# Optimization experiments

Measured on AMD Instinct MI355X. Metric: run time of the kernel, lower is better.

The kernel has to match this reference:

```python
import jax, jax.numpy as jnp
import numpy as np

LEAK = 0.1

def _l2n(x):
    return x / (jnp.linalg.norm(x) + 1e-12)

def _sn_weight(W, u):
    # torch spectral_norm: one power iteration from buffer u, u/v detached,
    # grad flows through W via sigma = u' W v.
    v = jax.lax.stop_gradient(_l2n(W.T @ u))
    u2 = jax.lax.stop_gradient(_l2n(W @ v))
    sigma = u2 @ (W @ v)
    return W / sigma

def _conv1x1(x, W, b):
    # x: (B,C,H,W), W: (O,C) -> (B,O,H,W)
    return jnp.einsum('oc,bchw->bohw', W, x) + b[None, :, None, None]

def _sn_layer(x, W, b, u):
    return jax.nn.leaky_relu(_conv1x1(x, _sn_weight(W, u), b), LEAK)

def _attention(x, qW, qb, kW, kb, vW, vb, gamma):
    B, C, H, Wd = x.shape
    N = H * Wd
    q = _conv1x1(x, qW, qb).reshape(B, -1, N)   # (B, C//8, N)
    k = _conv1x1(x, kW, kb).reshape(B, -1, N)   # (B, C//8, N)
    v = _conv1x1(x, vW, vb).reshape(B, C, N)    # (B, C, N)
    # energy[b,n,m] = sum_c q[b,c,n] * k[b,c,m]  (query^T key)
    energy = jnp.einsum('bcn,bcm->bnm', q, k)
    amap = jax.nn.softmax(energy, axis=-1)
    # aw[b,c,m] = sum_n v[b,c,n] * amap[b,m,n]   (bmm(v, amap^T))
    aw = jnp.einsum('bcn,bmn->bcm', v, amap).reshape(B, C, H, Wd)
    return gamma * aw + x


def setup_inputs() -> dict:
    key = jax.random.key(0)
    ks = iter(jax.random.split(key, 64))
    def nrm(shape, s=0.05):
        return jax.random.normal(next(ks), shape, jnp.float32) * s
    d = {'input': jax.random.normal(next(ks), (4, 6, 64, 64), jnp.float32)}
    dims = [(6, 64), (64, 128), (128, 256), (256, 512), (512, 1)]
    for i, (cin, cout) in enumerate(dims, 1):
        d[f'W{i}'] = nrm((cout, cin))
        d[f'b{i}'] = nrm((cout,))
        d[f'u{i}'] = _l2n(jax.random.normal(next(ks), (cout,), jnp.float32))
    for tag, C in (('a1', 256), ('a2', 512)):
        d[f'{tag}_qW'] = nrm((C // 8, C)); d[f'{tag}_qb'] = nrm((C // 8,))
        d[f'{tag}_kW'] = nrm((C // 8, C)); d[f'{tag}_kb'] = nrm((C // 8,))
        d[f'{tag}_vW'] = nrm((C, C));      d[f'{tag}_vb'] = nrm((C,))
        d[f'{tag}_gamma'] = jnp.full((1,), 0.1, jnp.float32)
    return d


def reference(input, W1, b1, u1, W2, b2, u2, W3, b3, u3, W4, b4, u4, W5, b5, u5,
              a1_qW, a1_qb, a1_kW, a1_kb, a1_vW, a1_vb, a1_gamma,
              a2_qW, a2_qb, a2_kW, a2_kb, a2_vW, a2_vb, a2_gamma):
    out = _sn_layer(input, W1, b1, u1)
    out = _sn_layer(out, W2, b2, u2)
    out = _sn_layer(out, W3, b3, u3)
    out = _attention(out, a1_qW, a1_qb, a1_kW, a1_kb, a1_vW, a1_vb, a1_gamma)
    out = _sn_layer(out, W4, b4, u4)
    out = _attention(out, a2_qW, a2_qb, a2_kW, a2_kb, a2_vW, a2_vb, a2_gamma)
    out = _sn_layer(out, W5, b5, u5)
    return out.squeeze()  # (B, H, W)
```

## Files before the change

### kernel.cpp

```cpp
#include <hip/hip_runtime.h>
#include <math.h>

#define N_PIX 4096
#define BATCH 4
#define LOG2E 1.4426950408889634f

typedef __bf16 bf16x8 __attribute__((ext_vector_type(8)));
typedef __bf16 bf16x4v __attribute__((ext_vector_type(4)));
typedef float f32x4 __attribute__((ext_vector_type(4)));

__device__ __forceinline__ unsigned pack4_fp8(float a, float b, float c, float d) {
    unsigned p = __builtin_amdgcn_cvt_pk_fp8_f32(a, b, 0, false);
    p = __builtin_amdgcn_cvt_pk_fp8_f32(c, d, p, true);
    return p;
}
__device__ __forceinline__ uint8_t to_fp8(float v) {
    return (uint8_t)(__builtin_amdgcn_cvt_pk_fp8_f32(v, v, 0, false) & 0xff);
}

struct SigP {
    const float* W[5];
    const float* u[5];
    int O[5];
    int C[5];
};

__device__ __forceinline__ void sig_map(int bid, int& L, int& ch) {
    if (bid == 0)      { L = 0; ch = 0; }
    else if (bid < 3)  { L = 1; ch = bid - 1; }
    else if (bid < 7)  { L = 2; ch = bid - 3; }
    else if (bid < 15) { L = 3; ch = bid - 7; }
    else               { L = 4; ch = 0; }
}

__global__ __launch_bounds__(256)
void sigma_p1(SigP p, float* __restrict__ ybuf) {
    __shared__ float ush[64];
    int L, ch;
    sig_map(blockIdx.x, L, ch);
    const float* W = p.W[L];
    const float* u = p.u[L];
    int O = p.O[L], C = p.C[L];
    int o0 = ch * 64;
    int no = O - o0; if (no > 64) no = 64;
    int t = threadIdx.x;
    if (t < 64) ush[t] = (t < no) ? u[o0 + t] : 0.f;
    __syncthreads();
    for (int c = t; c < C; c += 256) {
        float a = 0.f;
        for (int o = 0; o < no; ++o) a += W[(size_t)(o0 + o) * C + c] * ush[o];
        atomicAdd(&ybuf[L * 512 + c], a);
    }
}

__global__ __launch_bounds__(256)
void sigma_p2(SigP p, const float* __restrict__ ybuf,
              float* __restrict__ S1, float* __restrict__ S2) {
    __shared__ float ysh[512];
    int L, ch;
    sig_map(blockIdx.x, L, ch);
    const float* W = p.W[L];
    int O = p.O[L], C = p.C[L];
    int o0 = ch * 64;
    int o_hi = o0 + 64; if (o_hi > O) o_hi = O;
    int t = threadIdx.x;
    int lane = t & 63, w = t >> 6;
    for (int c = t; c < C; c += 256) ysh[c] = ybuf[L * 512 + c];
    __syncthreads();

    if (ch == 0) {
        float s = 0.f;
        for (int c = t; c < C; c += 256) s += ysh[c] * ysh[c];
        #pragma unroll
        for (int off = 1; off < 64; off <<= 1) s += __shfl_xor(s, off);
        if (lane == 0) atomicAdd(&S1[L], s);
    }

    float sq = 0.f;
    for (int i = 0; i < 16; ++i) {
        int o = o0 + w * 16 + i;
        if (o >= o_hi) break;
        float a = 0.f;
        for (int c = lane; c < C; c += 64) a += W[(size_t)o * C + c] * ysh[c];
        #pragma unroll
        for (int off = 1; off < 64; off <<= 1) a += __shfl_xor(a, off);
        if (lane == 0) sq += a * a;
    }
    if (lane == 0) atomicAdd(&S2[L], sq);
}

__global__ __launch_bounds__(256)
void wsplit_kernel(const float* __restrict__ W, const float* __restrict__ iv,
                   float scale, int C, __bf16* __restrict__ out) {
    int o = blockIdx.x;
    float s = (iv ? iv[0] : 1.f) * scale;
    for (int c = threadIdx.x; c < C; c += 256) {
        float wv = W[(size_t)o * C + c] * s;
        __bf16 hi = (__bf16)wv;
        float lo = wv - (float)hi;
        out[(size_t)o * 2 * C + c] = hi;
        out[(size_t)o * 2 * C + C + c] = (__bf16)lo;
    }
}

__global__ __launch_bounds__(256)
void concat_bias(const float* __restrict__ qb1, const float* __restrict__ kb1,
                 const float* __restrict__ qb2, const float* __restrict__ kb2,
                 float* __restrict__ bb,
                 const float* __restrict__ S1, const float* __restrict__ S2,
                 float* __restrict__ sig) {
    int t = threadIdx.x;
    if (t < 32) bb[t] = qb1[t] * LOG2E;
    else if (t < 64) bb[t] = kb1[t - 32];
    else if (t < 128) bb[t] = qb2[t - 64] * LOG2E;
    else if (t < 192) bb[t] = kb2[t - 128];
    else if (t >= 224 && t < 229) {
        int L = t - 224;
        float rinv = 1.f / (sqrtf(S1[L]) + 1e-12f);
        float ns2 = rinv * rinv * S2[L];
        float sg = ns2 / (sqrtf(ns2) + 1e-12f);
        sig[L] = 1.f / sg;
    }
}

__global__ __launch_bounds__(256)
void conv_f32_kernel(const float* __restrict__ x, const float* __restrict__ W,
                     const float* __restrict__ bias, const float* __restrict__ sig,
                     float* __restrict__ out, int C, int O, int lrelu) {
    __shared__ float Ws[16][68];
    __shared__ float Xs[16][68];
    int t = threadIdx.x;
    int tx = t & 15, ty = t >> 4;
    int b = blockIdx.z;
    int n0 = blockIdx.x * 64, o0 = blockIdx.y * 64;
    float acc[4][4] = {};
    const float* xb = x + (size_t)b * C * N_PIX;
    for (int c0 = 0; c0 < C; c0 += 16) {
        #pragma unroll
        for (int i = 0; i < 4; ++i) {
            int e = t + i * 256;
            int o = e >> 4, c = e & 15;
            float wv = 0.f;
            if (o0 + o < O && c0 + c < C) wv = W[(size_t)(o0 + o) * C + c0 + c];
            Ws[c][o] = wv;
        }
        #pragma unroll
        for (int i = 0; i < 4; ++i) {
            int e = t + i * 256;
            int c = e >> 6, n = e & 63;
            float xv = 0.f;
            if (c0 + c < C) xv = xb[(size_t)(c0 + c) * N_PIX + n0 + n];
            Xs[c][n] = xv;
        }
        __syncthreads();
        #pragma unroll
        for (int cc = 0; cc < 16; ++cc) {
            float4 wv = *(const float4*)&Ws[cc][ty * 4];
            float4 xv = *(const float4*)&Xs[cc][tx * 4];
            float wa[4] = {wv.x, wv.y, wv.z, wv.w};
            float xa[4] = {xv.x, xv.y, xv.z, xv.w};
            #pragma unroll
            for (int i = 0; i < 4; ++i)
                #pragma unroll
                for (int j = 0; j < 4; ++j)
                    acc[i][j] += wa[i] * xa[j];
        }
        __syncthreads();
    }
    float ivv = sig ? sig[0] : 1.f;
    for (int i = 0; i < 4; ++i) {
        int o = o0 + ty * 4 + i;
        if (o >= O) break;
        float bv = bias[o];
        float vres[4];
        #pragma unroll
        for (int j = 0; j < 4; ++j) {
            float v = acc[i][j] * ivv + bv;
            if (lrelu) v = (v > 0.f) ? v : 0.1f * v;
            vres[j] = v;
        }
        *(float4*)&out[((size_t)b * O + o) * N_PIX + n0 + tx * 4] =
            make_float4(vres[0], vres[1], vres[2], vres[3]);
    }
}

__global__ __launch_bounds__(256)
void tsplit64_kernel(const float* __restrict__ in, __bf16* __restrict__ out) {
    __shared__ float tile[64 * 65];
    int t = threadIdx.x;
    int n0 = blockIdx.x * 64, b = blockIdx.y;
    for (int e = t; e < 64 * 64; e += 256) {
        int c = e >> 6, n = e & 63;
        tile[n * 65 + c] = in[((size_t)b * 64 + c) * N_PIX + n0 + n];
    }
    __syncthreads();
    for (int e = t; e < 64 * 64; e += 256) {
        int n = e >> 6, c = e & 63;
        float v = tile[n * 65 + c];
        __bf16 hi = (__bf16)v;
        size_t base = ((size_t)b * N_PIX + n0 + n) * 128;
        out[base + c] = hi;
        out[base + 64 + c] = (__bf16)(v - (float)hi);
    }
}

template <int WO, int WN, int MF, int MODE, int IN_F32, int LRELU>
__global__ __launch_bounds__(256)
void mfma_conv(const void* __restrict__ xt, const __bf16* __restrict__ wsp,
               const float* __restrict__ bias, float bscale,
               void* __restrict__ outp, int C, int O) {
    constexpr int NT_BLK = WN * 128;
    constexpr int OT_BLK = WO * 16 * MF;
    __shared__ __bf16 Ws[OT_BLK * 72];
    __shared__ __bf16 Xs[NT_BLK * 72];
    int t = threadIdx.x;
    int lane = t & 63, w = t >> 6;
    int l15 = lane & 15, quad = lane >> 4;
    int wo = w / WN, wn = w % WN;
    int b = blockIdx.z;
    int n0b = blockIdx.x * NT_BLK, o0b = blockIdx.y * OT_BLK;

    f32x4 acc[MF][8] = {};

    for (int c0 = 0; c0 < C; c0 += 32) {
        __syncthreads();
        for (int e = t; e < OT_BLK * 8; e += 256) {
            int row = e >> 3, part = e & 7;
            size_t src = (size_t)(o0b + row) * 2 * C +
                         (part < 4 ? c0 + part * 8 : C + c0 + (part - 4) * 8);
            int dst = row * 72 + (part < 4 ? part * 8 : 32 + (part - 4) * 8);
            *(uint4*)&Ws[dst] = *(const uint4*)&wsp[src];
        }
        if (IN_F32) {
            const float* xf = (const float*)xt;
            for (int e = t; e < NT_BLK * 8; e += 256) {
                int row = e >> 3, part = e & 7;
                float4 v = *(const float4*)&xf[((size_t)b * N_PIX + n0b + row) * C + c0 + part * 4];
                bf16x4v hi, lo;
                float va[4] = {v.x, v.y, v.z, v.w};
                #pragma unroll
                for (int j = 0; j < 4; ++j) {
                    hi[j] = (__bf16)va[j];
                    lo[j] = (__bf16)(va[j] - (float)hi[j]);
                }
                *(bf16x4v*)&Xs[row * 72 + part * 4] = hi;
                *(bf16x4v*)&Xs[row * 72 + 32 + part * 4] = lo;
            }
        } else {
            const __bf16* xb = (const __bf16*)xt;
            for (int e = t; e < NT_BLK * 8; e += 256) {
                int row = e >> 3, part = e & 7;
                size_t src = ((size_t)b * N_PIX + n0b + row) * 2 * C +
                             (part < 4 ? c0 + part * 8 : C + c0 + (part - 4) * 8);
                int dst = row * 72 + (part < 4 ? part * 8 : 32 + (part - 4) * 8);
                *(uint4*)&Xs[dst] = *(const uint4*)&xb[src];
            }
        }
        __syncthreads();

        bf16x8 ah[MF], al[MF];
        #pragma unroll
        for (int mf = 0; mf < MF; ++mf) {
            int base = (wo * 16 * MF + mf * 16 + l15) * 72 + quad * 8;
            ah[mf] = *(const bf16x8*)&Ws[base];
            al[mf] = *(const bf16x8*)&Ws[base + 32];
        }
        #pragma unroll
        for (int nt = 0; nt < 8; ++nt) {
            int bbase = (wn * 128 + nt * 16 + l15) * 72 + quad * 8;
            bf16x8 bh = *(const bf16x8*)&Xs[bbase];
            bf16x8 bl = *(const bf16x8*)&Xs[bbase + 32];
            #pragma unroll
            for (int mf = 0; mf < MF; ++mf) {
                acc[mf][nt] = __builtin_amdgcn_mfma_f32_16x16x32_bf16(ah[mf], bh, acc[mf][nt], 0, 0, 0);
                acc[mf][nt] = __builtin_amdgcn_mfma_f32_16x16x32_bf16(ah[mf], bl, acc[mf][nt], 0, 0, 0);
                acc[mf][nt] = __builtin_amdgcn_mfma_f32_16x16x32_bf16(al[mf], bh, acc[mf][nt], 0, 0, 0);
            }
        }
    }

    float bv[MF][4];
    #pragma unroll
    for (int mf = 0; mf < MF; ++mf)
        #pragma unroll
        for (int r = 0; r < 4; ++r)
            bv[mf][r] = bias[o0b + wo * 16 * MF + mf * 16 + quad * 4 + r] * bscale;

    #pragma unroll
    for (int mf = 0; mf < MF; ++mf)
        #pragma unroll
        for (int nt = 0; nt < 8; ++nt) {
            int n = n0b + wn * 128 + nt * 16 + l15;
            float val[4];
            #pragma unroll
            for (int r = 0; r < 4; ++r) {
                float v = acc[mf][nt][r] + bv[mf][r];
                if (LRELU) v = (v > 0.f) ? v : 0.1f * v;
                val[r] = v;
            }
            int obase = o0b + wo * 16 * MF + mf * 16 + quad * 4;
            if (MODE == 1) {
                uint8_t* ob = (uint8_t*)outp;
                #pragma unroll
                for (int r = 0; r < 4; ++r)
                    ob[((size_t)b * O + obase + r) * N_PIX + n] = to_fp8(val[r]);
            } else if (MODE == 2) {
                __bf16* ob = (__bf16*)outp;
                bf16x4v hv, lv;
                #pragma unroll
                for (int r = 0; r < 4; ++r) {
                    hv[r] = (__bf16)val[r];
                    lv[r] = (__bf16)(val[r] - (float)hv[r]);
                }
                size_t rb = ((size_t)b * N_PIX + n) * 2 * O + obase;
                *(bf16x4v*)&ob[rb] = hv;
                *(bf16x4v*)&ob[rb + O] = lv;
            } else {
                __bf16* ob = (__bf16*)outp;
                bf16x4v hv;
                #pragma unroll
                for (int r = 0; r < 4; ++r) hv[r] = (__bf16)val[r];
                *(bf16x4v*)&ob[((size_t)b * N_PIX + n) * O + obase] = hv;
            }
        }
}

template <int CQ, int KITER>
__global__ __launch_bounds__(256)
void s_gemm3(const __bf16* __restrict__ qt, const __bf16* __restrict__ kt,
             uint8_t* __restrict__ S, int QSTR) {
    constexpr int NKK = CQ / 32;
    __shared__ uint8_t Ss[2][128 * 144];
    int t = threadIdx.x;
    int lane = t & 63, w = t >> 6;
    int l15 = lane & 15, quad = lane >> 4;
    int kbase = blockIdx.x * KITER * 128, q0 = blockIdx.y * 128, b = blockIdx.z;

    bf16x8 qf[8][NKK];
    #pragma unroll
    for (int nt = 0; nt < 8; ++nt)
        #pragma unroll
        for (int kk = 0; kk < NKK; ++kk)
            qf[nt][kk] = *(const bf16x8*)&qt[((size_t)b * N_PIX + q0 + nt * 16 + l15) * QSTR + kk * 32 + quad * 8];

    for (int ki = 0; ki < KITER; ++ki) {
        int k0 = kbase + ki * 128;
        int cur = ki & 1;
        bf16x8 kf[2][NKK];
        #pragma unroll
        for (int mf = 0; mf < 2; ++mf)
            #pragma unroll
            for (int kk = 0; kk < NKK; ++kk)
                kf[mf][kk] = *(const bf16x8*)&kt[((size_t)b * N_PIX + k0 + w * 32 + mf * 16 + l15) * QSTR + kk * 32 + quad * 8];

        #pragma unroll
        for (int nt = 0; nt < 8; ++nt) {
            f32x4 a[2] = {};
            #pragma unroll
            for (int kk = 0; kk < NKK; ++kk)
                #pragma unroll
                for (int mf = 0; mf < 2; ++mf)
                    a[mf] = __builtin_amdgcn_mfma_f32_16x16x32_bf16(kf[mf][kk], qf[nt][kk], a[mf], 0, 0, 0);
            #pragma unroll
            for (int mf = 0; mf < 2; ++mf) {
                unsigned p = pack4_fp8(exp2f(a[mf][0]), exp2f(a[mf][1]),
                                       exp2f(a[mf][2]), exp2f(a[mf][3]));
                *(unsigned*)&Ss[cur][(nt * 16 + l15) * 144 + w * 32 + mf * 16 + quad * 4] = p;
            }
        }
        __syncthreads();
        int ql = t >> 1, kh = (t & 1) * 64;
        size_t row = ((size_t)b * N_PIX + q0 + ql) * (size_t)N_PIX + k0 + kh;
        #pragma unroll
        for (int j = 0; j < 4; ++j)
            *(uint4*)&S[row + j * 16] = *(const uint4*)&Ss[cur][ql * 144 + kh + j * 16];
    }
}

typedef __attribute__((address_space(1))) const void* gas1_t;
typedef __attribute__((address_space(3))) void* las3_t;

template <int NT, int QROWS>
__global__ __launch_bounds__(1024)
void pv_gemm13(const uint8_t* __restrict__ E, const uint8_t* __restrict__ vg,
               const __bf16* __restrict__ xin2,
               const float* __restrict__ gamma, float* __restrict__ out, int C) {
    constexpr int NQS = QROWS / 32;
    constexpr int NCS = 16 / NQS;
    constexpr int CCH = NT * 16 * NCS;
    constexpr int NPAIR = (N_PIX / QROWS) * BATCH;
    __shared__ uint8_t PshA[QROWS * 128];
    __shared__ uint8_t PshB[QROWS * 128];
    __shared__ uint8_t VshA[CCH * 128];
    __shared__ uint8_t VshB[CCH * 128];
    int t = threadIdx.x;
    int lane = t & 63, w = t >> 6;
    int l15 = lane & 15, quad = lane >> 4;
    int qs = w % NQS, cs = w / NQS;
    int bid = blockIdx.x;
    int pair = bid % NPAIR, cblk = bid / NPAIR;
    int qi = pair >> 2, b = pair & 3;
    int q0 = qi * QROWS, c0 = cblk * CCH;
    const uint8_t* Pb = E + ((size_t)b * N_PIX + q0) * (size_t)N_PIX;
    const uint8_t* Vb = vg + ((size_t)b * C + c0) * (size_t)N_PIX;

    int r8 = lane >> 3;
    int cgl = (lane & 7) ^ r8;

    const long ONES = 0x3838383838383838L;

    f32x4 acc[2][NT] = {};
    f32x4 acc_s[2] = {};

    auto stage = [&](uint8_t* Ps, uint8_t* Vs, int k0) {
        #pragma unroll
        for (int ch = 0; ch < QROWS / 128; ++ch) {
            int row0 = w * (QROWS / 16) + ch * 8;
            const uint8_t* g = Pb + (size_t)(row0 + r8) * N_PIX + k0 + cgl * 16;
            __builtin_amdgcn_global_load_lds((gas1_t)g, (las3_t)&Ps[row0 * 128], 16, 0, 0);
        }
        static_assert(CCH / 8 == 16, "V staging assumes 16 chunks");
        {
            int row0 = w * 8;
            const uint8_t* g = Vb + (size_t)(row0 + r8) * N_PIX + k0 + cgl * 16;
            __builtin_amdgcn_global_load_lds((gas1_t)g, (las3_t)&Vs[row0 * 128], 16, 0, 0);
        }
    };

    auto compute = [&](const uint8_t* Ps, const uint8_t* Vs) {
        #pragma unroll
        for (int kk = 0; kk < 4; ++kk) {
            long pa[2];
            #pragma unroll
            for (int mf = 0; mf < 2; ++mf) {
                int row = qs * 32 + mf * 16 + l15;
                int cg = (2 * kk + (quad >> 1)) ^ (row & 7);
                pa[mf] = *(const long*)&Ps[row * 128 + cg * 16 + (quad & 1) * 8];
            }
            #pragma unroll
            for (int mf = 0; mf < 2; ++mf)
                acc_s[mf] = __builtin_amdgcn_mfma_f32_16x16x32_fp8_fp8(pa[mf], ONES, acc_s[mf], 0, 0, 0);
            #pragma unroll
            for (int nt = 0; nt < NT; ++nt) {
                int row = cs * (NT * 16) + nt * 16 + l15;
                int cg = (2 * kk + (quad >> 1)) ^ (row & 7);
                long vf = *(const long*)&Vs[row * 128 + cg * 16 + (quad & 1) * 8];
                #pragma unroll
                for (int mf = 0; mf < 2; ++mf)
                    acc[mf][nt] = __builtin_amdgcn_mfma_f32_16x16x32_fp8_fp8(pa[mf], vf, acc[mf][nt], 0, 0, 0);
            }
        }
    };

    stage(PshA, VshA, 0);
    __syncthreads();

    for (int k0 = 0; k0 < N_PIX; k0 += 256) {
        stage(PshB, VshB, k0 + 128);
        compute(PshA, VshA);
        __syncthreads();
        if (k0 + 256 < N_PIX) stage(PshA, VshA, k0 + 256);
        compute(PshB, VshB);
        __syncthreads();
    }

    float g = gamma[0];
    #pragma unroll
    for (int mf = 0; mf < 2; ++mf)
        #pragma unroll
        for (int r = 0; r < 4; ++r) {
            int ql = qs * 32 + mf * 16 + quad * 4 + r;
            int q = q0 + ql;
            float gil = g / acc_s[mf][r];
            size_t xrb = ((size_t)b * N_PIX + q) * 2 * C;
            size_t orb = ((size_t)b * N_PIX + q) * C;
            #pragma unroll
            for (int nt = 0; nt < NT; ++nt) {
                int c = c0 + cs * (NT * 16) + nt * 16 + l15;
                float xr = (float)xin2[xrb + c] + (float)xin2[xrb + C + c];
                out[orb + c] = gil * acc[mf][nt][r] + xr;
            }
        }
}

__global__ __launch_bounds__(256)
void l5_kernel(const float* __restrict__ h, const float* __restrict__ W5,
               const float* __restrict__ b5, const float* __restrict__ sig,
               float* __restrict__ out) {
    int t = threadIdx.x;
    int lane = t & 63, w = t >> 6;
    int p = blockIdx.x * 4 + w;
    const float* row = h + (size_t)p * 512;
    float4 a0 = *(const float4*)&row[lane * 8];
    float4 a1 = *(const float4*)&row[lane * 8 + 4];
    float4 w0 = *(const float4*)&W5[lane * 8];
    float4 w1 = *(const float4*)&W5[lane * 8 + 4];
    float s = a0.x * w0.x + a0.y * w0.y + a0.z * w0.z + a0.w * w0.w +
              a1.x * w1.x + a1.y * w1.y + a1.z * w1.z + a1.w * w1.w;
    #pragma unroll
    for (int off = 1; off < 64; off <<= 1) s += __shfl_xor(s, off);
    if (lane == 0) {
        float v = sig[0] * s + b5[0];
        out[p] = (v > 0.f) ? v : 0.1f * v;
    }
}

extern "C" void kernel_launch(void* const* d_in, const int* in_sizes, int n_in,
                              void* d_out, int out_size, void* d_ws, size_t ws_size,
                              hipStream_t stream) {
    const float* x   = (const float*)d_in[0];
    const float* W1  = (const float*)d_in[1];
    const float* b1  = (const float*)d_in[2];
    const float* u1  = (const float*)d_in[3];
    const float* W2  = (const float*)d_in[4];
    const float* b2  = (const float*)d_in[5];
    const float* u2  = (const float*)d_in[6];
    const float* W3  = (const float*)d_in[7];
    const float* b3  = (const float*)d_in[8];
    const float* u3  = (const float*)d_in[9];
    const float* W4  = (const float*)d_in[10];
    const float* b4  = (const float*)d_in[11];
    const float* u4  = (const float*)d_in[12];
    const float* W5  = (const float*)d_in[13];
    const float* b5  = (const float*)d_in[14];
    const float* u5  = (const float*)d_in[15];
    const float* a1_qW = (const float*)d_in[16];
    const float* a1_qb = (const float*)d_in[17];
    const float* a1_kW = (const float*)d_in[18];
    const float* a1_kb = (const float*)d_in[19];
    const float* a1_vW = (const float*)d_in[20];
    const float* a1_vb = (const float*)d_in[21];
    const float* a1_g  = (const float*)d_in[22];
    const float* a2_qW = (const float*)d_in[23];
    const float* a2_qb = (const float*)d_in[24];
    const float* a2_kW = (const float*)d_in[25];
    const float* a2_kb = (const float*)d_in[26];
    const float* a2_vW = (const float*)d_in[27];
    const float* a2_vb = (const float*)d_in[28];
    const float* a2_g  = (const float*)d_in[29];

    float* ws = (float*)d_ws;
    const size_t NF = (size_t)BATCH * N_PIX;
    float* sig    = ws;
    float* h1     = ws + 16;
    float* slabC  = h1 + NF * 64;
    float* slabS1 = slabC + NF * 512;
    float* slabS2 = slabS1 + NF * 256;
    float* qtf    = slabS2 + NF * 512;
    float* ktf    = qtf + NF * 32;
    float* wspf   = ktf + NF * 32;
    float* bbf    = wspf + 592000;
    float* ysig   = wspf + 592256;
    float* Sf     = wspf + 600000;

    __bf16* h1t = (__bf16*)slabS1;
    __bf16* h2t = (__bf16*)slabS2;
    __bf16* h3t = (__bf16*)slabS1;
    __bf16* h5t = (__bf16*)slabS2;
    float*  h4t = slabC;
    uint8_t* vb1 = (uint8_t*)(slabC + NF * 256);
    float*  h6t = slabC;
    uint8_t* vb2 = (uint8_t*)slabS1;
    __bf16* qkt = (__bf16*)qtf;
    __bf16* wsp = (__bf16*)wspf;
    uint8_t* Sbuf = (uint8_t*)Sf;

    float* ybuf = ysig;
    float* S1v  = ysig + 2560;
    float* S2v  = ysig + 2576;

    __bf16* wsL2  = wsp;
    __bf16* wsL3  = wsL2 + 16384;
    __bf16* wsL4  = wsL3 + 65536;
    __bf16* wsA1q = wsL4 + 262144;
    __bf16* wsA1k = wsA1q + 16384;
    __bf16* wsA1v = wsA1k + 16384;
    __bf16* wsA2q = wsA1v + 131072;
    __bf16* wsA2k = wsA2q + 65536;
    __bf16* wsA2v = wsA2k + 65536;

    dim3 blk(256);

    SigP sp;
    sp.W[0] = W1; sp.u[0] = u1; sp.O[0] = 64;  sp.C[0] = 6;
    sp.W[1] = W2; sp.u[1] = u2; sp.O[1] = 128; sp.C[1] = 64;
    sp.W[2] = W3; sp.u[2] = u3; sp.O[2] = 256; sp.C[2] = 128;
    sp.W[3] = W4; sp.u[3] = u4; sp.O[3] = 512; sp.C[3] = 256;
    sp.W[4] = W5; sp.u[4] = u5; sp.O[4] = 1;   sp.C[4] = 512;

    hipMemsetAsync(ysig, 0, 2592 * sizeof(float), stream);
    sigma_p1<<<dim3(16), blk, 0, stream>>>(sp, ybuf);
    sigma_p2<<<dim3(16), blk, 0, stream>>>(sp, ybuf, S1v, S2v);
    concat_bias<<<1, blk, 0, stream>>>(a1_qb, a1_kb, a2_qb, a2_kb, bbf, S1v, S2v, sig);

    wsplit_kernel<<<128, blk, 0, stream>>>(W2, sig + 1, 1.f, 64, wsL2);
    wsplit_kernel<<<256, blk, 0, stream>>>(W3, sig + 2, 1.f, 128, wsL3);
    wsplit_kernel<<<512, blk, 0, stream>>>(W4, sig + 3, 1.f, 256, wsL4);
    wsplit_kernel<<<32,  blk, 0, stream>>>(a1_qW, nullptr, LOG2E, 256, wsA1q);
    wsplit_kernel<<<32,  blk, 0, stream>>>(a1_kW, nullptr, 1.f, 256, wsA1k);
    wsplit_kernel<<<256, blk, 0, stream>>>(a1_vW, nullptr, 1.f, 256, wsA1v);
    wsplit_kernel<<<64,  blk, 0, stream>>>(a2_qW, nullptr, LOG2E, 512, wsA2q);
    wsplit_kernel<<<64,  blk, 0, stream>>>(a2_kW, nullptr, 1.f, 512, wsA2k);
    wsplit_kernel<<<512, blk, 0, stream>>>(a2_vW, nullptr, 1.f, 512, wsA2v);

    conv_f32_kernel<<<dim3(64, 1, 4), blk, 0, stream>>>(x, W1, b1, sig + 0, h1, 6, 64, 1);
    tsplit64_kernel<<<dim3(64, 4), blk, 0, stream>>>(h1, h1t);

    mfma_conv<4, 1, 1, 2, 0, 1><<<dim3(32, 2, 4), blk, 0, stream>>>(h1t, wsL2, b2, 1.f, h2t, 64, 128);
    mfma_conv<4, 1, 1, 2, 0, 1><<<dim3(32, 4, 4), blk, 0, stream>>>(h2t, wsL3, b3, 1.f, h3t, 128, 256);

    mfma_conv<2, 2, 1, 4, 0, 0><<<dim3(16, 2, 4), blk, 0, stream>>>(h3t, wsA1q, bbf, 1.f, qkt, 256, 64);
    mfma_conv<4, 1, 1, 1, 0, 0><<<dim3(32, 4, 4), blk, 0, stream>>>(h3t, wsA1v, a1_vb, 1.f, vb1, 256, 256);
    s_gemm3<32, 8><<<dim3(4, 32, 4), blk, 0, stream>>>(qkt, qkt + 32, Sbuf, 64);
    pv_gemm13<2, 128><<<dim3(256), dim3(1024), 0, stream>>>(Sbuf, vb1, h3t, a1_g, h4t, 256);

    mfma_conv<4, 1, 1, 2, 1, 1><<<dim3(32, 8, 4), blk, 0, stream>>>(h4t, wsL4, b4, 1.f, h5t, 256, 512);

    mfma_conv<2, 2, 1, 4, 0, 0><<<dim3(16, 4, 4), blk, 0, stream>>>(h5t, wsA2q, bbf + 64, 1.f, qkt, 512, 128);
    mfma_conv<4, 1, 1, 1, 0, 0><<<dim3(32, 8, 4), blk, 0, stream>>>(h5t, wsA2v, a2_vb, 1.f, vb2, 512, 512);
    s_gemm3<64, 8><<<dim3(4, 32, 4), blk, 0, stream>>>(qkt, qkt + 64, Sbuf, 128);
    pv_gemm13<4, 256><<<dim3(256), dim3(1024), 0, stream>>>(Sbuf, vb2, h5t, a2_g, h6t, 512);

    l5_kernel<<<4096, blk, 0, stream>>>(h6t, W5, b5, sig + 4, (float*)d_out);
}
```

Baseline: 526.4 us.

## Batch weight-split launches, fuse conv1 with transpose-split, drop memset and atomics

Measured after the change: 505.7 us, median of 2. -3.9%, faster.

```diff
diff --git a/kernel.cpp b/kernel.cpp
--- a/kernel.cpp
+++ b/kernel.cpp
@@ -49,23 +49,31 @@
     for (int c = t; c < C; c += 256) {
         float a = 0.f;
         for (int o = 0; o < no; ++o) a += W[(size_t)(o0 + o) * C + c] * ush[o];
-        atomicAdd(&ybuf[L * 512 + c], a);
+        ybuf[(size_t)blockIdx.x * 512 + c] = a;
     }
 }
 
 __global__ __launch_bounds__(256)
 void sigma_p2(SigP p, const float* __restrict__ ybuf,
-              float* __restrict__ S1, float* __restrict__ S2) {
+              float* __restrict__ S1, float* __restrict__ S2p) {
     __shared__ float ysh[512];
+    __shared__ float red[8];
     int L, ch;
     sig_map(blockIdx.x, L, ch);
+    const int baseT[5] = {0, 1, 3, 7, 15};
+    const int cntT[5]  = {1, 2, 4, 8, 1};
+    int base = baseT[L], cnt = cntT[L];
     const float* W = p.W[L];
     int O = p.O[L], C = p.C[L];
     int o0 = ch * 64;
     int o_hi = o0 + 64; if (o_hi > O) o_hi = O;
     int t = threadIdx.x;
     int lane = t & 63, w = t >> 6;
-    for (int c = t; c < C; c += 256) ysh[c] = ybuf[L * 512 + c];
+    for (int c = t; c < C; c += 256) {
+        float s = 0.f;
+        for (int i = 0; i < cnt; ++i) s += ybuf[(size_t)(base + i) * 512 + c];
+        ysh[c] = s;
+    }
     __syncthreads();
 
     if (ch == 0) {
@@ -73,7 +81,7 @@
         for (int c = t; c < C; c += 256) s += ysh[c] * ysh[c];
         #pragma unroll
         for (int off = 1; off < 64; off <<= 1) s += __shfl_xor(s, off);
-        if (lane == 0) atomicAdd(&S1[L], s);
+        if (lane == 0) red[w] = s;
     }
 
     float sq = 0.f;
@@ -86,20 +94,40 @@
         for (int off = 1; off < 64; off <<= 1) a += __shfl_xor(a, off);
         if (lane == 0) sq += a * a;
     }
-    if (lane == 0) atomicAdd(&S2[L], sq);
-}
-
-__global__ __launch_bounds__(256)
-void wsplit_kernel(const float* __restrict__ W, const float* __restrict__ iv,
-                   float scale, int C, __bf16* __restrict__ out) {
-    int o = blockIdx.x;
-    float s = (iv ? iv[0] : 1.f) * scale;
+    if (lane == 0) red[4 + w] = sq;
+    __syncthreads();
+    if (t == 0) {
+        if (ch == 0) S1[L] = red[0] + red[1] + red[2] + red[3];
+        S2p[blockIdx.x] = red[4] + red[5] + red[6] + red[7];
+    }
+}
+
+struct WsAll {
+    const float* W[9];
+    __bf16* out[9];
+    int C[9];
+    int sigidx[9];
+    float scale[9];
+    int end[9];
+};
+
+__global__ __launch_bounds__(256)
+void wsplit_all(WsAll p, const float* __restrict__ sig) {
+    int bid = blockIdx.x;
+    int s = 0;
+    #pragma unroll
+    for (int i = 0; i < 9; ++i)
+        if (bid >= p.end[i]) s = i + 1;
+    int o = bid - (s ? p.end[s - 1] : 0);
+    const float* W = p.W[s];
+    __bf16* out = p.out[s];
+    int C = p.C[s];
+    float sc = (p.sigidx[s] >= 0 ? sig[p.sigidx[s]] : 1.f) * p.scale[s];
     for (int c = threadIdx.x; c < C; c += 256) {
-        float wv = W[(size_t)o * C + c] * s;
+        float wv = W[(size_t)o * C + c] * sc;
         __bf16 hi = (__bf16)wv;
-        float lo = wv - (float)hi;
         out[(size_t)o * 2 * C + c] = hi;
-        out[(size_t)o * 2 * C + C + c] = (__bf16)lo;
+        out[(size_t)o * 2 * C + C + c] = (__bf16)(wv - (float)hi);
     }
 }
 
@@ -107,7 +135,7 @@
 void concat_bias(const float* __restrict__ qb1, const float* __restrict__ kb1,
                  const float* __restrict__ qb2, const float* __restrict__ kb2,
                  float* __restrict__ bb,
-                 const float* __restrict__ S1, const float* __restrict__ S2,
+                 const float* __restrict__ S1, const float* __restrict__ S2p,
                  float* __restrict__ sig) {
     int t = threadIdx.x;
     if (t < 32) bb[t] = qb1[t] * LOG2E;
@@ -116,82 +144,69 @@
     else if (t < 192) bb[t] = kb2[t - 128];
     else if (t >= 224 && t < 229) {
         int L = t - 224;
+        const int baseT[5] = {0, 1, 3, 7, 15};
+        const int cntT[5]  = {1, 2, 4, 8, 1};
+        float s2 = 0.f;
+        for (int i = 0; i < cntT[L]; ++i) s2 += S2p[baseT[L] + i];
         float rinv = 1.f / (sqrtf(S1[L]) + 1e-12f);
-        float ns2 = rinv * rinv * S2[L];
+        float ns2 = rinv * rinv * s2;
         float sg = ns2 / (sqrtf(ns2) + 1e-12f);
         sig[L] = 1.f / sg;
     }
 }
 
 __global__ __launch_bounds__(256)
-void conv_f32_kernel(const float* __restrict__ x, const float* __restrict__ W,
-                     const float* __restrict__ bias, const float* __restrict__ sig,
-                     float* __restrict__ out, int C, int O, int lrelu) {
+void conv1_kernel(const float* __restrict__ x, const float* __restrict__ W,
+                  const float* __restrict__ bias, const float* __restrict__ sig,
+                  __bf16* __restrict__ out) {
+    constexpr int C = 6;
     __shared__ float Ws[16][68];
     __shared__ float Xs[16][68];
+    __shared__ float tile[64 * 65];
     int t = threadIdx.x;
     int tx = t & 15, ty = t >> 4;
     int b = blockIdx.z;
-    int n0 = blockIdx.x * 64, o0 = blockIdx.y * 64;
+    int n0 = blockIdx.x * 64;
     float acc[4][4] = {};
     const float* xb = x + (size_t)b * C * N_PIX;
-    for (int c0 = 0; c0 < C; c0 += 16) {
-        #pragma unroll
-        for (int i = 0; i < 4; ++i) {
-            int e = t + i * 256;
-            int o = e >> 4, c = e & 15;
-            float wv = 0.f;
-            if (o0 + o < O && c0 + c < C) wv = W[(size_t)(o0 + o) * C + c0 + c];
-            Ws[c][o] = wv;
-        }
-        #pragma unroll
-        for (int i = 0; i < 4; ++i) {
-            int e = t + i * 256;
-            int c = e >> 6, n = e & 63;
-            float xv = 0.f;
-            if (c0 + c < C) xv = xb[(size_t)(c0 + c) * N_PIX + n0 + n];
-            Xs[c][n] = xv;
-        }
-        __syncthreads();
-        #pragma unroll
-        for (int cc = 0; cc < 16; ++cc) {
-            float4 wv = *(const float4*)&Ws[cc][ty * 4];
-            float4 xv = *(const float4*)&Xs[cc][tx * 4];
-            float wa[4] = {wv.x, wv.y, wv.z, wv.w};
-            float xa[4] = {xv.x, xv.y, xv.z, xv.w};
-            #pragma unroll
-            for (int i = 0; i < 4; ++i)
-                #pragma unroll
-                for (int j = 0; j < 4; ++j)
-                    acc[i][j] += wa[i] * xa[j];
-        }
-        __syncthreads();
-    }
-    float ivv = sig ? sig[0] : 1.f;
+
+    #pragma unroll
     for (int i = 0; i < 4; ++i) {
-        int o = o0 + ty * 4 + i;
-        if (o >= O) break;
+        int e = t + i * 256;
+        int o = e >> 4, c = e & 15;
+        Ws[c][o] = (c < C) ? W[(size_t)o * C + c] : 0.f;
+    }
+    #pragma unroll
+    for (int i = 0; i < 4; ++i) {
+        int e = t + i * 256;
+        int c = e >> 6, n = e & 63;
+        Xs[c][n] = (c < C) ? xb[(size_t)c * N_PIX + n0 + n] : 0.f;
+    }
+    __syncthreads();
+    #pragma unroll
+    for (int cc = 0; cc < 16; ++cc) {
+        float4 wv = *(const float4*)&Ws[cc][ty * 4];
+        float4 xv = *(const float4*)&Xs[cc][tx * 4];
+        float wa[4] = {wv.x, wv.y, wv.z, wv.w};
+        float xa[4] = {xv.x, xv.y, xv.z, xv.w};
+        #pragma unroll
+        for (int i = 0; i < 4; ++i)
+            #pragma unroll
+            for (int j = 0; j < 4; ++j)
+                acc[i][j] += wa[i] * xa[j];
+    }
+
+    float ivv = sig[0];
+    #pragma unroll
+    for (int i = 0; i < 4; ++i) {
+        int o = ty * 4 + i;
         float bv = bias[o];
-        float vres[4];
         #pragma unroll
         for (int j = 0; j < 4; ++j) {
             float v = acc[i][j] * ivv + bv;
-            if (lrelu) v = (v > 0.f) ? v : 0.1f * v;
-            vres[j] = v;
-        }
-        *(float4*)&out[((size_t)b * O + o) * N_PIX + n0 + tx * 4] =
-            make_float4(vres[0], vres[1], vres[2], vres[3]);
-    }
-}
-
-__global__ __launch_bounds__(256)
-void tsplit64_kernel(const float* __restrict__ in, __bf16* __restrict__ out) {
-    __shared__ float tile[64 * 65];
-    int t = threadIdx.x;
-    int n0 = blockIdx.x * 64, b = blockIdx.y;
-    for (int e = t; e < 64 * 64; e += 256) {
-        int c = e >> 6, n = e & 63;
-        tile[n * 65 + c] = in[((size_t)b * 64 + c) * N_PIX + n0 + n];
+            v = (v > 0.f) ? v : 0.1f * v;
+            tile[(tx * 4 + j) * 65 + o] = v;
+        }
     }
     __syncthreads();
     for (int e = t; e < 64 * 64; e += 256) {
@@ -550,7 +565,6 @@
     float* ktf    = qtf + NF * 32;
     float* wspf   = ktf + NF * 32;
     float* bbf    = wspf + 592000;
-    float* ysig   = wspf + 592256;
     float* Sf     = wspf + 600000;
 
     __bf16* h1t = (__bf16*)slabS1;
@@ -565,9 +579,9 @@
     __bf16* wsp = (__bf16*)wspf;
     uint8_t* Sbuf = (uint8_t*)Sf;
 
-    float* ybuf = ysig;
-    float* S1v  = ysig + 2560;
-    float* S2v  = ysig + 2576;
+    float* ybuf = wspf + 582000;
+    float* S1v  = wspf + 590200;
+    float* S2p  = wspf + 590208;
 
     __bf16* wsL2  = wsp;
     __bf16* wsL3  = wsL2 + 16384;
@@ -588,23 +602,26 @@
     sp.W[3] = W4; sp.u[3] = u4; sp.O[3] = 512; sp.C[3] = 256;
     sp.W[4] = W5; sp.u[4] = u5; sp.O[4] = 1;   sp.C[4] = 512;
 
-    hipMemsetAsync(ysig, 0, 2592 * sizeof(float), stream);
     sigma_p1<<<dim3(16), blk, 0, stream>>>(sp, ybuf);
-    sigma_p2<<<dim3(16), blk, 0, stream>>>(sp, ybuf, S1v, S2v);
-    concat_bias<<<1, blk, 0, stream>>>(a1_qb, a1_kb, a2_qb, a2_kb, bbf, S1v, S2v, sig);
-
-    wsplit_kernel<<<128, blk, 0, stream>>>(W2, sig + 1, 1.f, 64, wsL2);
-    wsplit_kernel<<<256, blk, 0, stream>>>(W3, sig + 2, 1.f, 128, wsL3);
-    wsplit_kernel<<<512, blk, 0, stream>>>(W4, sig + 3, 1.f, 256, wsL4);
-    wsplit_kernel<<<32,  blk, 0, stream>>>(a1_qW, nullptr, LOG2E, 256, wsA1q);
-    wsplit_kernel<<<32,  blk, 0, stream>>>(a1_kW, nullptr, 1.f, 256, wsA1k);
-    wsplit_kernel<<<256, blk, 0, stream>>>(a1_vW, nullptr, 1.f, 256, wsA1v);
-    wsplit_kernel<<<64,  blk, 0, stream>>>(a2_qW, nullptr, LOG2E, 512, wsA2q);
-    wsplit_kernel<<<64,  blk, 0, stream>>>(a2_kW, nullptr, 1.f, 512, wsA2k);
-    wsplit_kernel<<<512, blk, 0, stream>>>(a2_vW, nullptr, 1.f, 512, wsA2v);
-
-    conv_f32_kernel<<<dim3(64, 1, 4), blk, 0, stream>>>(x, W1, b1, sig + 0, h1, 6, 64, 1);
-    tsplit64_kernel<<<dim3(64, 4), blk, 0, stream>>>(h1, h1t);
+    sigma_p2<<<dim3(16), blk, 0, stream>>>(sp, ybuf, S1v, S2p);
+    concat_bias<<<1, blk, 0, stream>>>(a1_qb, a1_kb, a2_qb, a2_kb, bbf, S1v, S2p, sig);
+
+    WsAll wa;
+    const float* wW[9]   = {W2, W3, W4, a1_qW, a1_kW, a1_vW, a2_qW, a2_kW, a2_vW};
+    __bf16* wO[9]        = {wsL2, wsL3, wsL4, wsA1q, wsA1k, wsA1v, wsA2q, wsA2k, wsA2v};
+    const int wC[9]      = {64, 128, 256, 256, 256, 256, 512, 512, 512};
+    const int wSig[9]    = {1, 2, 3, -1, -1, -1, -1, -1, -1};
+    const float wScl[9]  = {1.f, 1.f, 1.f, LOG2E, 1.f, 1.f, LOG2E, 1.f, 1.f};
+    const int wRows[9]   = {128, 256, 512, 32, 32, 256, 64, 64, 512};
+    int cum = 0;
+    for (int i = 0; i < 9; ++i) {
+        wa.W[i] = wW[i]; wa.out[i] = wO[i]; wa.C[i] = wC[i];
+        wa.sigidx[i] = wSig[i]; wa.scale[i] = wScl[i];
+        cum += wRows[i]; wa.end[i] = cum;
+    }
+    wsplit_all<<<dim3(cum), blk, 0, stream>>>(wa, sig);
+
+    conv1_kernel<<<dim3(64, 1, 4), blk, 0, stream>>>(x, W1, b1, sig, h1t);
 
     mfma_conv<4, 1, 1, 2, 0, 1><<<dim3(32, 2, 4), blk, 0, stream>>>(h1t, wsL2, b2, 1.f, h2t, 64, 128);
     mfma_conv<4, 1, 1, 2, 0, 1><<<dim3(32, 4, 4), blk, 0, stream>>>(h2t, wsL3, b3, 1.f, h3t, 128, 256);
```
